# Optimization experiments

Measured on AMD Instinct MI355X. Metric: run time of the kernel, lower is better.

The kernel has to match this reference:

```python
import jax, jax.numpy as jnp
import numpy as np

B, S, H, NH, G = 2, 2048, 2048, 16, 2
HD = H // NH          # head_dim = 128
NKV = NH // G         # kv heads = 8
EPS = 1e-6


def setup_inputs() -> dict:
    key = jax.random.key(0)
    ks = jax.random.split(key, 5)
    sc = 0.02
    return {
        "x": jax.random.normal(ks[0], (B, S, H), jnp.float32),
        "wq": jax.random.normal(ks[1], (H, H), jnp.float32) * sc,
        "wk": jax.random.normal(ks[2], (H, H // G), jnp.float32) * sc,
        "wv": jax.random.normal(ks[3], (H, H // G), jnp.float32) * sc,
        "wo": jax.random.normal(ks[4], (H, H), jnp.float32) * sc,
        "rms_w": jnp.ones((HD,), jnp.float32),
        "token_positions": jnp.arange(S, dtype=jnp.int32),
    }


def _rmsnorm(x, w):
    # x: (b, s, HD, n_heads); normalize over the head_dim axis (axis 2)
    ms = jnp.mean(x * x, axis=2, keepdims=True)
    return x * jax.lax.rsqrt(ms + EPS) * w[None, None, :, None]


def _rope(x, pos):
    # x: (b, s, HD, n); interleaved-pair rotation along HD, base 10000
    half = HD // 2
    inv_freq = 1.0 / (10000.0 ** (jnp.arange(half, dtype=jnp.float32) * 2.0 / HD))
    ang = pos.astype(jnp.float32)[:, None] * inv_freq[None, :]   # (s, HD/2)
    cos = jnp.cos(ang)[None, :, :, None]
    sin = jnp.sin(ang)[None, :, :, None]
    x1 = x[:, :, 0::2, :]
    x2 = x[:, :, 1::2, :]
    r1 = x1 * cos - x2 * sin
    r2 = x1 * sin + x2 * cos
    return jnp.stack([r1, r2], axis=3).reshape(x.shape)


def reference(x, wq, wk, wv, wo, rms_w, token_positions):
    b, s, _ = x.shape
    # projections, split hidden as (head_dim, n_heads) exactly like the torch .view
    q = (x @ wq).reshape(b, s, HD, NH)
    k = (x @ wk).reshape(b, s, HD, NKV)
    v = (x @ wv).reshape(b, s, HD, NKV)
    # per-head RMSNorm (over head_dim) then RoPE on Q and K
    q = _rope(_rmsnorm(q, rms_w), token_positions)
    k = _rope(_rmsnorm(k, rms_w), token_positions)
    # grouped-query attention: group G query heads per kv head
    q5 = q.reshape(b, s, HD, NKV, G)
    scores = jnp.einsum('bsdkg,btdk->bkgst', q5, k)          # (b,NKV,G,s,s)
    mask = jnp.triu(jnp.ones((s, s), bool), 1)               # causal
    scores = jnp.where(mask[None, None, None], -jnp.inf, scores)
    attn = jax.nn.softmax(scores / jnp.sqrt(jnp.float32(HD)), axis=-1)
    ctx = jnp.einsum('bkgst,btdk->bkgsd', attn, v)           # (b,NKV,G,s,HD)
    ctx = ctx.reshape(b, NH, s, HD).transpose(0, 2, 1, 3).reshape(b, s, H)
    return ctx @ wo
```

## Files before the change

kernel.cpp:

```cpp
#include <hip/hip_runtime.h>
#include <hip/hip_bf16.h>
#include <stdint.h>

typedef unsigned short u16;
typedef uint32_t u32;
typedef __attribute__((ext_vector_type(8))) short s8v;
typedef __attribute__((ext_vector_type(4))) float f4v;
typedef __attribute__((ext_vector_type(4))) unsigned int u4v;

#define SQ   2048
#define HDIM 2048
#define HD_  128
#define NH_  16
#define NKV_ 8

__device__ __forceinline__ u16 f2b(float f) {
  uint32_t u = __builtin_bit_cast(uint32_t, f);
  u += 0x7fffu + ((u >> 16) & 1u);
  return (u16)(u >> 16);
}
__device__ __forceinline__ float b2f(u16 v) {
  uint32_t u = ((uint32_t)v) << 16;
  return __builtin_bit_cast(float, u);
}
__device__ __forceinline__ u32 pk2(float lo, float hi) {
  return (u32)f2b(lo) | ((u32)f2b(hi) << 16);
}

__global__ __launch_bounds__(256) void k_cast(const float* __restrict__ in,
                                              u16* __restrict__ out, int n4) {
  int i = blockIdx.x * 256 + threadIdx.x;
  if (i >= n4) return;
  f4v v = *(const f4v*)(in + (size_t)i * 4);
  union { u16 s[4]; uint64_t u; } o;
  o.s[0] = f2b(v[0]); o.s[1] = f2b(v[1]); o.s[2] = f2b(v[2]); o.s[3] = f2b(v[3]);
  *(uint64_t*)(out + (size_t)i * 4) = o.u;
}

__global__ __launch_bounds__(256) void k_transpose4(const float* __restrict__ wq,
                                                    const float* __restrict__ wk,
                                                    const float* __restrict__ wv,
                                                    const float* __restrict__ wo,
                                                    u16* __restrict__ wqt,
                                                    u16* __restrict__ wkt,
                                                    u16* __restrict__ wvt,
                                                    u16* __restrict__ wot) {
  const int z = blockIdx.z;
  const float* in = (z == 0) ? wq : (z == 1) ? wk : (z == 2) ? wv : wo;
  u16* out = (z == 0) ? wqt : (z == 1) ? wkt : (z == 2) ? wvt : wot;
  const int cols = (z == 1 || z == 2) ? 1024 : 2048;
  int c0 = blockIdx.x * 32, r0 = blockIdx.y * 32;
  if (c0 >= cols) return;
  __shared__ float tile[32][33];
  int tx = threadIdx.x & 31, ty = threadIdx.x >> 5;
#pragma unroll
  for (int i = 0; i < 32; i += 8)
    tile[ty + i][tx] = in[(size_t)(r0 + ty + i) * cols + c0 + tx];
  __syncthreads();
#pragma unroll
  for (int i = 0; i < 32; i += 8)
    out[(size_t)(c0 + ty + i) * 2048 + r0 + tx] = f2b(tile[tx][ty + i]);
}

template <int F32OUT>
__global__ __launch_bounds__(256) void k_gemm(const u16* __restrict__ A,
                                              const u16* __restrict__ Bt,
                                              void* __restrict__ C,
                                              int M, int N, int K) {
  __shared__ __align__(16) u16 As[128 * 64];
  __shared__ __align__(16) u16 Bs[128 * 64];
  const int tid = threadIdx.x;
  const int lane = tid & 63, wvi = tid >> 6;
  const int wm = wvi >> 1, wn = wvi & 1;
  const int l15 = lane & 15, l4 = lane >> 4;
  const int m0 = blockIdx.y * 128, n0 = blockIdx.x * 128;
  auto* As3 = (__attribute__((address_space(3))) char*)As;
  auto* Bs3 = (__attribute__((address_space(3))) char*)Bs;
  int srow[4], soff[4];
#pragma unroll
  for (int i = 0; i < 4; i++) {
    int slot = wvi * 4096 + i * 1024 + lane * 16;
    int r = slot >> 7;
    int gc = ((slot >> 4) & 7) ^ (r & 7);
    srow[i] = r; soff[i] = gc * 16;
  }
  f4v acc[4][4] = {};
  for (int k0 = 0; k0 < K; k0 += 64) {
#pragma unroll
    for (int i = 0; i < 4; i++) {
      const char* gA = (const char*)(A + (size_t)(m0 + srow[i]) * K + k0) + soff[i];
      const char* gB = (const char*)(Bt + (size_t)(n0 + srow[i]) * K + k0) + soff[i];
      __builtin_amdgcn_global_load_lds((__attribute__((address_space(1))) void*)gA,
                                       (__attribute__((address_space(3))) void*)(As3 + wvi * 4096 + i * 1024),
                                       16, 0, 0);
      __builtin_amdgcn_global_load_lds((__attribute__((address_space(1))) void*)gB,
                                       (__attribute__((address_space(3))) void*)(Bs3 + wvi * 4096 + i * 1024),
                                       16, 0, 0);
    }
    __syncthreads();
#pragma unroll
    for (int kk = 0; kk < 2; kk++) {
      s8v af[4], bf[4];
#pragma unroll
      for (int i = 0; i < 4; i++) {
        int ra = wm * 64 + i * 16 + l15;
        af[i] = *(const s8v*)((const char*)As + ra * 128 +
                              ((kk * 64 + l4 * 16) ^ ((ra & 7) << 4)));
        int rb = wn * 64 + i * 16 + l15;
        bf[i] = *(const s8v*)((const char*)Bs + rb * 128 +
                              ((kk * 64 + l4 * 16) ^ ((rb & 7) << 4)));
      }
#pragma unroll
      for (int i = 0; i < 4; i++)
#pragma unroll
        for (int j = 0; j < 4; j++)
          acc[i][j] = __builtin_amdgcn_mfma_f32_16x16x32_bf16(af[i], bf[j], acc[i][j], 0, 0, 0);
    }
    __syncthreads();
  }
#pragma unroll
  for (int i = 0; i < 4; i++) {
#pragma unroll
    for (int j = 0; j < 4; j++) {
      int mb = m0 + wm * 64 + i * 16 + l4 * 4;
      int nn = n0 + wn * 64 + j * 16 + l15;
#pragma unroll
      for (int r = 0; r < 4; r++) {
        float v = acc[i][j][r];
        if (F32OUT) ((float*)C)[(size_t)(mb + r) * N + nn] = v;
        else        ((u16*)C)[(size_t)(mb + r) * N + nn]  = f2b(v);
      }
    }
  }
}

__global__ __launch_bounds__(256) void k_normrope(const u16* __restrict__ qkv,
                                                  const float* __restrict__ rms_w,
                                                  const int* __restrict__ pos_arr,
                                                  u16* __restrict__ qq,
                                                  u16* __restrict__ kko,
                                                  u16* __restrict__ vto) {
  int idx = blockIdx.x;
  int b = idx >> 11, s = idx & 2047;
  int t = threadIdx.x;
  __shared__ float part[256];
  __shared__ float rstdq[16], rstdk[8];
  __shared__ float lcos[64], lsin[64];
  float pos = (float)pos_arr[s];
  if (t < 64) {
    float ang = pos * exp2f(-0.20762050593046f * (float)t);
    float sn, cs;
    sincosf(ang, &sn, &cs);
    lcos[t] = cs; lsin[t] = sn;
  }
  const u16* qr = qkv + (size_t)idx * 4096;
  const u16* kr = qr + 2048;
  const u16* vr = qr + 3072;
  int h = t & 15, ch = t >> 4;
  float qv[8]; float ss = 0.f;
#pragma unroll
  for (int j = 0; j < 8; j++) {
    float v = b2f(qr[(ch * 8 + j) * 16 + h]);
    qv[j] = v; ss += v * v;
  }
  part[t] = ss;
  __syncthreads();
  if (t < 16) {
    float tot = 0.f;
#pragma unroll
    for (int c = 0; c < 16; c++) tot += part[c * 16 + t];
    rstdq[t] = rsqrtf(tot * (1.f / 128.f) + 1e-6f);
  }
  __syncthreads();
  {
    float rs = rstdq[h];
    s8v ov;
#pragma unroll
    for (int p = 0; p < 4; p++) {
      int d0 = ch * 8 + p * 2;
      float v0 = qv[p * 2]     * rs * rms_w[d0];
      float v1 = qv[p * 2 + 1] * rs * rms_w[d0 + 1];
      float cs = lcos[d0 >> 1], sn = lsin[d0 >> 1];
      ov[p * 2]     = (short)f2b((v0 * cs - v1 * sn) * 0.08838834764831845f);
      ov[p * 2 + 1] = (short)f2b((v0 * sn + v1 * cs) * 0.08838834764831845f);
    }
    *(s8v*)(qq + ((size_t)(b * 16 + h) * SQ + s) * HD_ + ch * 8) = ov;
  }
  __syncthreads();
  int kv = t & 7, ch2 = t >> 3;
  float kvs[8]; float ssk = 0.f;
  if (t < 128) {
#pragma unroll
    for (int j = 0; j < 8; j++) {
      float v = b2f(kr[(ch2 * 8 + j) * 8 + kv]);
      kvs[j] = v; ssk += v * v;
    }
    part[t] = ssk;
  }
  __syncthreads();
  if (t < 8) {
    float tot = 0.f;
#pragma unroll
    for (int c = 0; c < 16; c++) tot += part[c * 8 + t];
    rstdk[t] = rsqrtf(tot * (1.f / 128.f) + 1e-6f);
  }
  __syncthreads();
  if (t < 128) {
    float rs = rstdk[kv];
    s8v ov;
#pragma unroll
    for (int p = 0; p < 4; p++) {
      int d0 = ch2 * 8 + p * 2;
      float v0 = kvs[p * 2]     * rs * rms_w[d0];
      float v1 = kvs[p * 2 + 1] * rs * rms_w[d0 + 1];
      float cs = lcos[d0 >> 1], sn = lsin[d0 >> 1];
      ov[p * 2]     = (short)f2b(v0 * cs - v1 * sn);
      ov[p * 2 + 1] = (short)f2b(v0 * sn + v1 * cs);
    }
    *(s8v*)(kko + ((size_t)(b * 8 + kv) * SQ + s) * HD_ + ch2 * 8) = ov;
#pragma unroll
    for (int j = 0; j < 8; j++) {
      int d = ch2 * 8 + j;
      vto[((size_t)(b * 8 + kv) * HD_ + d) * SQ + s] = vr[d * 8 + kv];
    }
  }
}

__global__ __launch_bounds__(256, 3) void k_attn(const u16* __restrict__ qq,
                                                 const u16* __restrict__ kk,
                                                 const u16* __restrict__ vt,
                                                 u16* __restrict__ ctx) {
  const int tile = (blockIdx.z == 1) ? (31 - (int)blockIdx.x) : (int)blockIdx.x;
  const int s0 = tile * 64;
  const int h  = blockIdx.y;
  const int b  = blockIdx.z;
  const int kvh = h >> 1;
  const int tid = threadIdx.x, lane = tid & 63, w = tid >> 6;
  const int l15 = lane & 15, l4 = lane >> 4;
  __shared__ __align__(16) u16 Kl[2][32 * 128];
  __shared__ __align__(16) u16 Vl[2][128 * 32];
  auto* K3 = (__attribute__((address_space(3))) char*)&Kl[0][0];
  auto* V3 = (__attribute__((address_space(3))) char*)&Vl[0][0];
  const u16* qbase = qq + (size_t)(b * 16 + h) * SQ * HD_;
  const u16* kbase = kk + (size_t)(b * 8 + kvh) * SQ * HD_;
  const u16* vbase = vt + (size_t)(b * 8 + kvh) * HD_ * SQ;
  const int swp = s0 + w * 16;

  int ksr[2], kso[2], vsr[2], vso[2];
#pragma unroll
  for (int j = 0; j < 2; j++) {
    int s = j * 256 + tid;
    ksr[j] = s >> 4;
    kso[j] = (((s & 15) ^ (ksr[j] & 7)) << 4);
    vsr[j] = s >> 2;
    vso[j] = (((s & 3) ^ ((vsr[j] >> 1) & 3)) << 4);
  }

  s8v qf[4];
#pragma unroll
  for (int c = 0; c < 4; c++)
    qf[c] = *(const s8v*)(qbase + (size_t)(swp + l15) * HD_ + c * 32 + l4 * 8);

  f4v o[8] = {};
  float m2 = -1e30f, l2 = 0.f;

  const int src1 = ((l4 & 1) << 5) + l15;
  const int src2 = src1 + 16;
  const bool lo = (l4 < 2);

  const int blockBound = s0 + 64;
  const int mybound = swp + 16;

#define STAGE(buf, t0s)                                                          \
  do {                                                                           \
    _Pragma("unroll")                                                            \
    for (int j = 0; j < 2; j++) {                                                \
      const char* gk = (const char*)(kbase + (size_t)((t0s) + ksr[j]) * HD_) + kso[j]; \
      __builtin_amdgcn_global_load_lds(                                          \
          (const __attribute__((address_space(1))) void*)gk,                     \
          (__attribute__((address_space(3))) void*)(K3 + (buf) * 8192 + j * 4096 + w * 1024 + (lane << 4)), \
          16, 0, 0);                                                             \
    }                                                                            \
    _Pragma("unroll")                                                            \
    for (int j = 0; j < 2; j++) {                                                \
      const char* gv = (const char*)(vbase + (size_t)vsr[j] * SQ + (t0s)) + vso[j]; \
      __builtin_amdgcn_global_load_lds(                                          \
          (const __attribute__((address_space(1))) void*)gv,                     \
          (__attribute__((address_space(3))) void*)(V3 + (buf) * 8192 + j * 4096 + w * 1024 + (lane << 4)), \
          16, 0, 0);                                                             \
    }                                                                            \
  } while (0)

  STAGE(0, 0);
  __syncthreads();
  int cur = 0;
  for (int t0 = 0; t0 < blockBound; t0 += 32) {
    if (t0 + 32 < blockBound) STAGE(cur ^ 1, t0 + 32);
    if (t0 < mybound) {
      const char* kbuf = (const char*)&Kl[cur][0];
      const char* vbuf = (const char*)&Vl[cur][0];
      s8v kf[2][4];
#pragma unroll
      for (int tt = 0; tt < 2; tt++) {
        int row = tt * 16 + l15;
#pragma unroll
        for (int c = 0; c < 4; c++)
          kf[tt][c] = *(const s8v*)(kbuf + row * 256 + ((((c << 2) + l4) ^ (row & 7)) << 4));
      }
      f4v sc[2] = {};
      __builtin_amdgcn_s_setprio(1);
#pragma unroll
      for (int tt = 0; tt < 2; tt++)
#pragma unroll
        for (int c = 0; c < 4; c++)
          sc[tt] = __builtin_amdgcn_mfma_f32_16x16x32_bf16(kf[tt][c], qf[c], sc[tt], 0, 0, 0);
      __builtin_amdgcn_s_setprio(0);
      if (t0 + 31 >= swp) {
#pragma unroll
        for (int tt = 0; tt < 2; tt++)
#pragma unroll
          for (int r = 0; r < 4; r++) {
            int tg = t0 + tt * 16 + l4 * 4 + r;
            int sg = swp + l15;
            if (tg > sg) sc[tt][r] = -1e30f;
          }
      }
      float mx = fmaxf(fmaxf(fmaxf(sc[0][0], sc[0][1]), fmaxf(sc[0][2], sc[0][3])),
                       fmaxf(fmaxf(sc[1][0], sc[1][1]), fmaxf(sc[1][2], sc[1][3])));
      mx = fmaxf(mx, __shfl_xor(mx, 16));
      mx = fmaxf(mx, __shfl_xor(mx, 32));
      if (__any(mx > m2 + 8.f)) {
        float mn = fmaxf(m2, mx);
        float sf = exp2f((m2 - mn) * 1.44269504f);
        m2 = mn; l2 *= sf;
#pragma unroll
        for (int dd = 0; dd < 8; dd++)
#pragma unroll
          for (int r = 0; r < 4; r++) o[dd][r] *= sf;
      }
      float p0[4], p1[4], sum = 0.f;
#pragma unroll
      for (int r = 0; r < 4; r++) {
        p0[r] = exp2f((sc[0][r] - m2) * 1.44269504f);
        p1[r] = exp2f((sc[1][r] - m2) * 1.44269504f);
        sum += p0[r] + p1[r];
      }
      sum += __shfl_xor(sum, 16);
      sum += __shfl_xor(sum, 32);
      l2 += sum;
      u32 pa = pk2(p0[0], p0[1]), pb = pk2(p0[2], p0[3]);
      u32 pc = pk2(p1[0], p1[1]), pd = pk2(p1[2], p1[3]);
      u32 xa1 = (u32)__shfl((int)pa, src1), xc1 = (u32)__shfl((int)pc, src1);
      u32 xb1 = (u32)__shfl((int)pb, src1), xd1 = (u32)__shfl((int)pd, src1);
      u32 xa2 = (u32)__shfl((int)pa, src2), xc2 = (u32)__shfl((int)pc, src2);
      u32 xb2 = (u32)__shfl((int)pb, src2), xd2 = (u32)__shfl((int)pd, src2);
      u4v fr;
      fr[0] = lo ? xa1 : xc1;
      fr[1] = lo ? xb1 : xd1;
      fr[2] = lo ? xa2 : xc2;
      fr[3] = lo ? xb2 : xd2;
      s8v pf = __builtin_bit_cast(s8v, fr);
      __builtin_amdgcn_s_setprio(1);
#pragma unroll
      for (int dd = 0; dd < 8; dd++) {
        int row = dd * 16 + l15;
        s8v vf = *(const s8v*)(vbuf + row * 64 + ((l4 ^ ((row >> 1) & 3)) << 4));
        o[dd] = __builtin_amdgcn_mfma_f32_16x16x32_bf16(vf, pf, o[dd], 0, 0, 0);
      }
      __builtin_amdgcn_s_setprio(0);
    }
    __syncthreads();
    cur ^= 1;
  }
#undef STAGE
  float inv = 1.f / l2;
  size_t rowoff = ((size_t)(b * SQ + swp + l15)) * HDIM + h * HD_;
#pragma unroll
  for (int dd = 0; dd < 8; dd++) {
    *(u32*)(ctx + rowoff + dd * 16 + l4 * 4)     = pk2(o[dd][0] * inv, o[dd][1] * inv);
    *(u32*)(ctx + rowoff + dd * 16 + l4 * 4 + 2) = pk2(o[dd][2] * inv, o[dd][3] * inv);
  }
}

extern "C" void kernel_launch(void* const* d_in, const int* in_sizes, int n_in,
                              void* d_out, int out_size, void* d_ws, size_t ws_size,
                              hipStream_t stream) {
  const float* x     = (const float*)d_in[0];
  const float* wq    = (const float*)d_in[1];
  const float* wk    = (const float*)d_in[2];
  const float* wv    = (const float*)d_in[3];
  const float* wo    = (const float*)d_in[4];
  const float* rms_w = (const float*)d_in[5];
  const int*   pos   = (const int*)d_in[6];

  u16* w = (u16*)d_ws;
  u16* xb   = w;
  u16* wqt  = xb   + 8388608;
  u16* wkt  = wqt  + 4194304;
  u16* wvt  = wkt  + 2097152;
  u16* wot  = wvt  + 2097152;
  u16* qkvraw = wot + 4194304;
  u16* kkb  = qkvraw + 16777216;
  u16* vtb  = kkb  + 4194304;
  u16* qqb  = wqt;
  u16* ctxb = xb;

  k_cast<<<8192, 256, 0, stream>>>(x, xb, 2097152);
  k_transpose4<<<dim3(64, 64, 4), 256, 0, stream>>>(wq, wk, wv, wo, wqt, wkt, wvt, wot);

  k_gemm<0><<<dim3(32, 32), 256, 0, stream>>>(xb, wqt, qkvraw, 4096, 4096, 2048);

  k_normrope<<<4096, 256, 0, stream>>>(qkvraw, rms_w, pos, qqb, kkb, vtb);

  k_attn<<<dim3(32, 16, 2), 256, 0, stream>>>(qqb, kkb, vtb, ctxb);

  k_gemm<1><<<dim3(16, 32), 256, 0, stream>>>(ctxb, wot, d_out, 4096, 2048, 2048);
}
```

Baseline: 286.0 us.

## Enlarge attention tiles to 128 queries and 64-key chunks with deeper prefetch

The attention kernel now uses 512-thread blocks covering 128 query rows each and processes 64-key K/V chunks. Each chunk load is shared across eight waves, which roughly halves global K/V traffic per query, and the score/PV loops issue twice as many MFMAs per synchronization. The pipeline now starts with two stages in flight and waits with explicit vmcnt plus raw barriers instead of __syncthreads. P is converted with the hardware v_cvt_pk_bf16_f32 instruction. The costs are twice the LDS, fewer blocks, and more causal-mask waste on diagonal tiles.

```diff
diff --git a/kernel.cpp b/kernel.cpp
--- a/kernel.cpp
+++ b/kernel.cpp
@@ -25,6 +25,11 @@
 }
 __device__ __forceinline__ u32 pk2(float lo, float hi) {
   return (u32)f2b(lo) | ((u32)f2b(hi) << 16);
+}
+__device__ __forceinline__ u32 cvtpk(float lo, float hi) {
+  u32 r;
+  asm("v_cvt_pk_bf16_f32 %0, %1, %2" : "=v"(r) : "v"(lo), "v"(hi));
+  return r;
 }
 
 __global__ __launch_bounds__(256) void k_cast(const float* __restrict__ in,
@@ -226,35 +231,54 @@
   }
 }
 
-__global__ __launch_bounds__(256, 3) void k_attn(const u16* __restrict__ qq,
+__global__ __launch_bounds__(512, 2) void k_attn(const u16* __restrict__ qq,
                                                  const u16* __restrict__ kk,
                                                  const u16* __restrict__ vt,
                                                  u16* __restrict__ ctx) {
-  const int tile = (blockIdx.z == 1) ? (31 - (int)blockIdx.x) : (int)blockIdx.x;
-  const int s0 = tile * 64;
+  const int tile = (blockIdx.z == 1) ? (15 - (int)blockIdx.x) : (int)blockIdx.x;
+  const int s0 = tile * 128;
   const int h  = blockIdx.y;
   const int b  = blockIdx.z;
   const int kvh = h >> 1;
   const int tid = threadIdx.x, lane = tid & 63, w = tid >> 6;
   const int l15 = lane & 15, l4 = lane >> 4;
-  __shared__ __align__(16) u16 Kl[2][32 * 128];
-  __shared__ __align__(16) u16 Vl[2][128 * 32];
+  __shared__ __align__(16) u16 Kl[2][64 * 128];
+  __shared__ __align__(16) u16 Vl[2][128 * 64];
   auto* K3 = (__attribute__((address_space(3))) char*)&Kl[0][0];
   auto* V3 = (__attribute__((address_space(3))) char*)&Vl[0][0];
   const u16* qbase = qq + (size_t)(b * 16 + h) * SQ * HD_;
   const u16* kbase = kk + (size_t)(b * 8 + kvh) * SQ * HD_;
   const u16* vbase = vt + (size_t)(b * 8 + kvh) * HD_ * SQ;
   const int swp = s0 + w * 16;
-
-  int ksr[2], kso[2], vsr[2], vso[2];
+  const int mybound = swp + 16;
+  const int ntiles = 2 * tile + 2;
+
+  int krow[2], kgo[2], vrow[2], vgo[2];
 #pragma unroll
   for (int j = 0; j < 2; j++) {
-    int s = j * 256 + tid;
-    ksr[j] = s >> 4;
-    kso[j] = (((s & 15) ^ (ksr[j] & 7)) << 4);
-    vsr[j] = s >> 2;
-    vso[j] = (((s & 3) ^ ((vsr[j] >> 1) & 3)) << 4);
-  }
+    int s = j * 8192 + tid * 16;
+    krow[j] = s >> 8;
+    kgo[j]  = (((s >> 4) & 15) ^ (krow[j] & 7)) * 8;
+    vrow[j] = s >> 7;
+    vgo[j]  = (((s >> 4) & 7) ^ (vrow[j] & 7)) * 8;
+  }
+
+#define STAGE(buf, t0s)                                                           \
+  do {                                                                            \
+    _Pragma("unroll")                                                             \
+    for (int j = 0; j < 2; j++) {                                                 \
+      const u16* gk = kbase + (size_t)((t0s) + krow[j]) * HD_ + kgo[j];           \
+      __builtin_amdgcn_global_load_lds(                                           \
+          (const __attribute__((address_space(1))) void*)gk,                      \
+          (__attribute__((address_space(3))) void*)(K3 + (buf) * 16384 + j * 8192 + tid * 16), \
+          16, 0, 0);                                                              \
+      const u16* gv = vbase + (size_t)vrow[j] * SQ + (t0s) + vgo[j];              \
+      __builtin_amdgcn_global_load_lds(                                           \
+          (const __attribute__((address_space(1))) void*)gv,                      \
+          (__attribute__((address_space(3))) void*)(V3 + (buf) * 16384 + j * 8192 + tid * 16), \
+          16, 0, 0);                                                              \
+    }                                                                             \
+  } while (0)
 
   s8v qf[4];
 #pragma unroll
@@ -266,67 +290,54 @@
 
   const int src1 = ((l4 & 1) << 5) + l15;
   const int src2 = src1 + 16;
-  const bool lo = (l4 < 2);
-
-  const int blockBound = s0 + 64;
-  const int mybound = swp + 16;
-
-#define STAGE(buf, t0s)                                                          \
-  do {                                                                           \
-    _Pragma("unroll")                                                            \
-    for (int j = 0; j < 2; j++) {                                                \
-      const char* gk = (const char*)(kbase + (size_t)((t0s) + ksr[j]) * HD_) + kso[j]; \
-      __builtin_amdgcn_global_load_lds(                                          \
-          (const __attribute__((address_space(1))) void*)gk,                     \
-          (__attribute__((address_space(3))) void*)(K3 + (buf) * 8192 + j * 4096 + w * 1024 + (lane << 4)), \
-          16, 0, 0);                                                             \
-    }                                                                            \
-    _Pragma("unroll")                                                            \
-    for (int j = 0; j < 2; j++) {                                                \
-      const char* gv = (const char*)(vbase + (size_t)vsr[j] * SQ + (t0s)) + vso[j]; \
-      __builtin_amdgcn_global_load_lds(                                          \
-          (const __attribute__((address_space(1))) void*)gv,                     \
-          (__attribute__((address_space(3))) void*)(V3 + (buf) * 8192 + j * 4096 + w * 1024 + (lane << 4)), \
-          16, 0, 0);                                                             \
-    }                                                                            \
-  } while (0)
+  const bool selhi = (l4 >> 1) != 0;
+  const int swzk = (l15 & 7);
+
+  int xk[4], xv[2];
+#pragma unroll
+  for (int c = 0; c < 4; c++) xk[c] = ((c * 4 + l4) ^ swzk) * 8;
+#pragma unroll
+  for (int ks = 0; ks < 2; ks++) xv[ks] = ((ks * 4 + l4) ^ swzk) * 8;
 
   STAGE(0, 0);
-  __syncthreads();
+  STAGE(1, 64);
   int cur = 0;
-  for (int t0 = 0; t0 < blockBound; t0 += 32) {
-    if (t0 + 32 < blockBound) STAGE(cur ^ 1, t0 + 32);
+  for (int i = 0; i < ntiles; i++) {
+    const int t0 = i * 64;
+    asm volatile("s_waitcnt vmcnt(4)" ::: "memory");
+    __builtin_amdgcn_s_barrier();
+    __builtin_amdgcn_sched_barrier(0);
     if (t0 < mybound) {
-      const char* kbuf = (const char*)&Kl[cur][0];
-      const char* vbuf = (const char*)&Vl[cur][0];
-      s8v kf[2][4];
-#pragma unroll
-      for (int tt = 0; tt < 2; tt++) {
-        int row = tt * 16 + l15;
-#pragma unroll
-        for (int c = 0; c < 4; c++)
-          kf[tt][c] = *(const s8v*)(kbuf + row * 256 + ((((c << 2) + l4) ^ (row & 7)) << 4));
-      }
-      f4v sc[2] = {};
+      const u16* kb = &Kl[cur][0];
+      const u16* vb = &Vl[cur][0];
+      f4v sc[4] = {};
       __builtin_amdgcn_s_setprio(1);
 #pragma unroll
-      for (int tt = 0; tt < 2; tt++)
-#pragma unroll
-        for (int c = 0; c < 4; c++)
-          sc[tt] = __builtin_amdgcn_mfma_f32_16x16x32_bf16(kf[tt][c], qf[c], sc[tt], 0, 0, 0);
+      for (int tt = 0; tt < 4; tt++) {
+        s8v kf0 = *(const s8v*)(kb + (tt * 16 + l15) * 128 + xk[0]);
+        s8v kf1 = *(const s8v*)(kb + (tt * 16 + l15) * 128 + xk[1]);
+        s8v kf2 = *(const s8v*)(kb + (tt * 16 + l15) * 128 + xk[2]);
+        s8v kf3 = *(const s8v*)(kb + (tt * 16 + l15) * 128 + xk[3]);
+        sc[tt] = __builtin_amdgcn_mfma_f32_16x16x32_bf16(kf0, qf[0], sc[tt], 0, 0, 0);
+        sc[tt] = __builtin_amdgcn_mfma_f32_16x16x32_bf16(kf1, qf[1], sc[tt], 0, 0, 0);
+        sc[tt] = __builtin_amdgcn_mfma_f32_16x16x32_bf16(kf2, qf[2], sc[tt], 0, 0, 0);
+        sc[tt] = __builtin_amdgcn_mfma_f32_16x16x32_bf16(kf3, qf[3], sc[tt], 0, 0, 0);
+      }
       __builtin_amdgcn_s_setprio(0);
-      if (t0 + 31 >= swp) {
-#pragma unroll
-        for (int tt = 0; tt < 2; tt++)
+      if (t0 + 63 > swp) {
+#pragma unroll
+        for (int tt = 0; tt < 4; tt++)
 #pragma unroll
           for (int r = 0; r < 4; r++) {
             int tg = t0 + tt * 16 + l4 * 4 + r;
-            int sg = swp + l15;
-            if (tg > sg) sc[tt][r] = -1e30f;
+            if (tg > swp + l15) sc[tt][r] = -1e30f;
           }
       }
-      float mx = fmaxf(fmaxf(fmaxf(sc[0][0], sc[0][1]), fmaxf(sc[0][2], sc[0][3])),
-                       fmaxf(fmaxf(sc[1][0], sc[1][1]), fmaxf(sc[1][2], sc[1][3])));
+      float mx = sc[0][0];
+#pragma unroll
+      for (int tt = 0; tt < 4; tt++)
+#pragma unroll
+        for (int r = 0; r < 4; r++) mx = fmaxf(mx, sc[tt][r]);
       mx = fmaxf(mx, __shfl_xor(mx, 16));
       mx = fmaxf(mx, __shfl_xor(mx, 32));
       if (__any(mx > m2 + 8.f)) {
@@ -338,38 +349,52 @@
 #pragma unroll
           for (int r = 0; r < 4; r++) o[dd][r] *= sf;
       }
-      float p0[4], p1[4], sum = 0.f;
-#pragma unroll
-      for (int r = 0; r < 4; r++) {
-        p0[r] = exp2f((sc[0][r] - m2) * 1.44269504f);
-        p1[r] = exp2f((sc[1][r] - m2) * 1.44269504f);
-        sum += p0[r] + p1[r];
+      u32 pk[4][2];
+      float sum = 0.f;
+#pragma unroll
+      for (int tt = 0; tt < 4; tt++) {
+        float p0 = exp2f((sc[tt][0] - m2) * 1.44269504f);
+        float p1 = exp2f((sc[tt][1] - m2) * 1.44269504f);
+        float p2 = exp2f((sc[tt][2] - m2) * 1.44269504f);
+        float p3 = exp2f((sc[tt][3] - m2) * 1.44269504f);
+        sum += (p0 + p1) + (p2 + p3);
+        pk[tt][0] = cvtpk(p0, p1);
+        pk[tt][1] = cvtpk(p2, p3);
       }
       sum += __shfl_xor(sum, 16);
       sum += __shfl_xor(sum, 32);
       l2 += sum;
-      u32 pa = pk2(p0[0], p0[1]), pb = pk2(p0[2], p0[3]);
-      u32 pc = pk2(p1[0], p1[1]), pd = pk2(p1[2], p1[3]);
-      u32 xa1 = (u32)__shfl((int)pa, src1), xc1 = (u32)__shfl((int)pc, src1);
-      u32 xb1 = (u32)__shfl((int)pb, src1), xd1 = (u32)__shfl((int)pd, src1);
-      u32 xa2 = (u32)__shfl((int)pa, src2), xc2 = (u32)__shfl((int)pc, src2);
-      u32 xb2 = (u32)__shfl((int)pb, src2), xd2 = (u32)__shfl((int)pd, src2);
-      u4v fr;
-      fr[0] = lo ? xa1 : xc1;
-      fr[1] = lo ? xb1 : xd1;
-      fr[2] = lo ? xa2 : xc2;
-      fr[3] = lo ? xb2 : xd2;
-      s8v pf = __builtin_bit_cast(s8v, fr);
+      s8v pf[2];
+#pragma unroll
+      for (int ks = 0; ks < 2; ks++) {
+        u32 e00 = (u32)__shfl((int)pk[2 * ks][0], src1);
+        u32 e01 = (u32)__shfl((int)pk[2 * ks][1], src1);
+        u32 e10 = (u32)__shfl((int)pk[2 * ks + 1][0], src1);
+        u32 e11 = (u32)__shfl((int)pk[2 * ks + 1][1], src1);
+        u32 f00 = (u32)__shfl((int)pk[2 * ks][0], src2);
+        u32 f01 = (u32)__shfl((int)pk[2 * ks][1], src2);
+        u32 f10 = (u32)__shfl((int)pk[2 * ks + 1][0], src2);
+        u32 f11 = (u32)__shfl((int)pk[2 * ks + 1][1], src2);
+        u4v fr;
+        fr[0] = selhi ? e10 : e00;
+        fr[1] = selhi ? e11 : e01;
+        fr[2] = selhi ? f10 : f00;
+        fr[3] = selhi ? f11 : f01;
+        pf[ks] = __builtin_bit_cast(s8v, fr);
+      }
       __builtin_amdgcn_s_setprio(1);
 #pragma unroll
       for (int dd = 0; dd < 8; dd++) {
-        int row = dd * 16 + l15;
-        s8v vf = *(const s8v*)(vbuf + row * 64 + ((l4 ^ ((row >> 1) & 3)) << 4));
-        o[dd] = __builtin_amdgcn_mfma_f32_16x16x32_bf16(vf, pf, o[dd], 0, 0, 0);
+        s8v vf0 = *(const s8v*)(vb + (dd * 16 + l15) * 64 + xv[0]);
+        s8v vf1 = *(const s8v*)(vb + (dd * 16 + l15) * 64 + xv[1]);
+        o[dd] = __builtin_amdgcn_mfma_f32_16x16x32_bf16(vf0, pf[0], o[dd], 0, 0, 0);
+        o[dd] = __builtin_amdgcn_mfma_f32_16x16x32_bf16(vf1, pf[1], o[dd], 0, 0, 0);
       }
       __builtin_amdgcn_s_setprio(0);
     }
-    __syncthreads();
+    __builtin_amdgcn_sched_barrier(0);
+    __builtin_amdgcn_s_barrier();
+    if (i + 2 < ntiles) STAGE(cur, t0 + 128);
     cur ^= 1;
   }
 #undef STAGE
@@ -377,8 +402,8 @@
   size_t rowoff = ((size_t)(b * SQ + swp + l15)) * HDIM + h * HD_;
 #pragma unroll
   for (int dd = 0; dd < 8; dd++) {
-    *(u32*)(ctx + rowoff + dd * 16 + l4 * 4)     = pk2(o[dd][0] * inv, o[dd][1] * inv);
-    *(u32*)(ctx + rowoff + dd * 16 + l4 * 4 + 2) = pk2(o[dd][2] * inv, o[dd][3] * inv);
+    *(u32*)(ctx + rowoff + dd * 16 + l4 * 4)     = cvtpk(o[dd][0] * inv, o[dd][1] * inv);
+    *(u32*)(ctx + rowoff + dd * 16 + l4 * 4 + 2) = cvtpk(o[dd][2] * inv, o[dd][3] * inv);
   }
 }
 
@@ -412,7 +437,7 @@
 
   k_normrope<<<4096, 256, 0, stream>>>(qkvraw, rms_w, pos, qqb, kkb, vtb);
 
-  k_attn<<<dim3(32, 16, 2), 256, 0, stream>>>(qqb, kkb, vtb, ctxb);
+  k_attn<<<dim3(16, 16, 2), 512, 0, stream>>>(qqb, kkb, vtb, ctxb);
 
   k_gemm<1><<<dim3(16, 32), 256, 0, stream>>>(ctxb, wot, d_out, 4096, 2048, 2048);
 }
```

Measured after the change: 270.9 us. -5.3%, faster.
